# Kernel tuning notes

Measured on AMD Instinct MI355X. Metric: run time of the kernel, lower is better.

Reference implementation:

```python
import jax, jax.numpy as jnp
import numpy as np

B, S, C, H, D = 2, 2048, 1024, 16, 64  # hidden C must equal H*D (value is a reshape of key_states)


def setup_inputs() -> dict:
    key = jax.random.key(0)
    ks = jax.random.split(key, 7)
    query_states = jax.random.normal(ks[0], (B, S, C), dtype=jnp.float32)
    key_states = jax.random.normal(ks[1], (B, S, C), dtype=jnp.float32)
    attention_mask = jax.random.randint(ks[2], (B, 1, 1, S), 0, 2).astype(jnp.int32)
    Wq = jax.random.normal(ks[3], (C, H, D), dtype=jnp.float32) * 0.02
    bq = jnp.zeros((H, D), dtype=jnp.float32)
    Wk = jax.random.normal(ks[4], (C, H, D), dtype=jnp.float32) * 0.02
    bk = jnp.zeros((H, D), dtype=jnp.float32)
    return {
        "query_states": query_states,
        "key_states": key_states,
        "attention_mask": attention_mask,
        "Wq": Wq,
        "bq": bq,
        "Wk": Wk,
        "bk": bk,
    }


def reference(query_states, key_states, attention_mask, Wq, bq, Wk, bk):
    # EinsumDense 'abc,cde->abde' with bias on 'de'
    q = jnp.einsum("bsc,chd->bshd", query_states, Wq) + bq  # [B,S,H,D]
    k = jnp.einsum("bsc,chd->bshd", key_states, Wk) + bk    # [B,S,H,D]
    # value is just key_states reshaped into head layout (no projection!)
    v = key_states.reshape(k.shape)                          # [B,S,H,D]
    # scale query by 1/sqrt(dk)
    q = q * jax.lax.rsqrt(jnp.asarray(D, q.dtype))
    # 'aecd,abcd->acbe': a=batch, c=head, b=query pos, e=key pos
    scores = jnp.einsum("bkhd,bqhd->bhqk", k, q)             # [B,H,Sq,Sk]
    mask = (1.0 - attention_mask.astype(scores.dtype)) * -10000.0
    scores = scores + mask
    probs = jax.nn.softmax(scores, axis=-1)
    # dropout is identity at training=False (default)
    # 'acbe,aecd->abcd': weighted sum of values over key positions
    out = jnp.einsum("bhqk,bkhd->bqhd", probs, v)            # [B,S,H,D]
    return out
```

## Files before the change

### kernel.cpp

```cpp
#include <hip/hip_runtime.h>

#define BSZ 2
#define SEQ 2048
#define CH  1024
#define NH  16
#define HD  64
#define LOG2E 1.4426950408889634f
#define MASKC (-14426.950408889634f)

typedef short  bf16x8 __attribute__((ext_vector_type(8)));
typedef short  bf16x4 __attribute__((ext_vector_type(4)));
typedef float  f32x4  __attribute__((ext_vector_type(4)));

__device__ __forceinline__ short f2bf(float f) {
    union { float f; unsigned u; } v; v.f = f;
    unsigned r = v.u + 0x7FFFu + ((v.u >> 16) & 1u);
    return (short)(r >> 16);
}
__device__ __forceinline__ short f2bf_fast(float f) {
    union { float f; unsigned u; } v; v.f = f;
    return (short)((v.u + 0x8000u) >> 16);
}
__device__ __forceinline__ float exp2_hw(float x) {
#if __has_builtin(__builtin_amdgcn_exp2f)
    return __builtin_amdgcn_exp2f(x);
#else
    float r;
    asm volatile("v_exp_f32 %0, %1\n\ts_nop 1" : "=v"(r) : "v"(x));
    return r;
#endif
}

#if __has_builtin(__builtin_amdgcn_mfma_f32_16x16x16bf16_1k)
__device__ __forceinline__ f32x4 mfma16x16x16(bf16x4 a, bf16x4 b, f32x4 c) {
    return __builtin_amdgcn_mfma_f32_16x16x16bf16_1k(a, b, c, 0, 0, 0);
}
#else
__device__ __forceinline__ f32x4 mfma16x16x16(bf16x4 a, bf16x4 b, f32x4 c) {
    f32x4 d;
    asm("v_mfma_f32_16x16x16_bf16 %0, %1, %2, %3"
        : "=v"(d) : "v"(a), "v"(b), "v"(c));
    return d;
}
#endif

__global__ __launch_bounds__(256) void prep(
    const float* __restrict__ query, const float* __restrict__ key,
    const float* __restrict__ Wq, const float* __restrict__ Wk,
    short* __restrict__ qc, short* __restrict__ kc,
    short* __restrict__ wtq, short* __restrict__ wtk,
    short* __restrict__ vtr)
{
    __shared__ float tile[64][65];
    const int bid = blockIdx.x;
    const int tid = threadIdx.x;

    if (bid < 4096) {
        const float* s = (bid < 2048) ? query : key;
        short*       d = (bid < 2048) ? qc : kc;
        long i = ((long)(bid & 2047) * 256 + tid) * 8;
        float4 v0 = *(const float4*)&s[i];
        float4 v1 = *(const float4*)&s[i + 4];
        bf16x8 o;
        o[0] = f2bf(v0.x); o[1] = f2bf(v0.y); o[2] = f2bf(v0.z); o[3] = f2bf(v0.w);
        o[4] = f2bf(v1.x); o[5] = f2bf(v1.y); o[6] = f2bf(v1.z); o[7] = f2bf(v1.w);
        *(bf16x8*)&d[i] = o;
        return;
    }

    const float* s; short* d;
    int r0, c0, srs, drs;
    if (bid < 4608) {
        int t = bid - 4096;
        s   = (t < 256) ? Wq : Wk;
        d   = (t < 256) ? wtq : wtk;
        t  &= 255;
        r0  = (t >> 4) * 64;
        c0  = (t & 15) * 64;
        srs = CH; drs = CH;
    } else {
        int t = bid - 4608;
        int z = t >> 5;
        int sy = t & 31;
        s   = key + (long)(z >> 4) * SEQ * CH + (long)(z & 15) * HD;
        d   = vtr + (long)z * HD * SEQ;
        r0  = sy * 64;
        c0  = 0;
        srs = CH; drs = SEQ;
    }

    const int r  = tid >> 2;
    const int c4 = (tid & 3) << 4;
    #pragma unroll
    for (int i = 0; i < 16; i += 4) {
        float4 v = *(const float4*)&s[(long)(r0 + r) * srs + c0 + c4 + i];
        tile[r][c4 + i + 0] = v.x;
        tile[r][c4 + i + 1] = v.y;
        tile[r][c4 + i + 2] = v.z;
        tile[r][c4 + i + 3] = v.w;
    }
    __syncthreads();
    bf16x8 o0, o1;
    #pragma unroll
    for (int i = 0; i < 8; i++) o0[i] = f2bf(tile[c4 + i][r]);
    #pragma unroll
    for (int i = 0; i < 8; i++) o1[i] = f2bf(tile[c4 + 8 + i][r]);
    *(bf16x8*)&d[(long)(c0 + r) * drs + r0 + c4 + 0] = o0;
    *(bf16x8*)&d[(long)(c0 + r) * drs + r0 + c4 + 8] = o1;
}

__global__ __launch_bounds__(256, 2) void proj_mfma(
    const short* __restrict__ Xq, const short* __restrict__ Xk,
    const short* __restrict__ Wtq, const short* __restrict__ Wtk,
    const float* __restrict__ bq_, const float* __restrict__ bk_,
    short* __restrict__ Yq, short* __restrict__ Yk)
{
    __shared__ short At[2][128 * 72];
    __shared__ short Bt[2][128 * 72];

    const int bid  = blockIdx.x;
    const int g    = bid >> 3, xcd = bid & 7;
    const int pair = ((g >> 3) << 3) | xcd;
    const int xt   = g & 7;
    const int yy   = pair >> 1;
    const int zz   = pair & 1;

    const short* X    = zz ? Xk  : Xq;
    const short* Wt   = zz ? Wtk : Wtq;
    const float* bias = zz ? bk_ : bq_;
    short*       Y    = zz ? Yk  : Yq;
    const float scale = zz ? 1.0f : (0.125f * LOG2E);

    const int tid  = threadIdx.x;
    const int lane = tid & 63, w = tid >> 6;
    const int quad = lane >> 4, t16 = lane & 15;
    const int m0 = yy * 128, n0 = xt * 128;
    const int srow = tid >> 1;
    const int shalf = (tid & 1) * 32;

    f32x4 acc[4][4];
    #pragma unroll
    for (int i = 0; i < 4; i++)
        #pragma unroll
        for (int j = 0; j < 4; j++)
            acc[i][j] = (f32x4){0.f, 0.f, 0.f, 0.f};

    const int M0 = (w >> 1) * 64, N0 = (w & 1) * 64;
    const int NIT = CH / 64;

    bf16x8 ar[4], br[4];
    #pragma unroll
    for (int c = 0; c < 4; c++) {
        ar[c] = *(const bf16x8*)&X [(long)(m0 + srow) * CH + shalf + 8 * c];
        br[c] = *(const bf16x8*)&Wt[(long)(n0 + srow) * CH + shalf + 8 * c];
    }
    #pragma unroll
    for (int c = 0; c < 4; c++) {
        *(bf16x8*)&At[0][srow * 72 + shalf + 8 * c] = ar[c];
        *(bf16x8*)&Bt[0][srow * 72 + shalf + 8 * c] = br[c];
    }
    #pragma unroll
    for (int c = 0; c < 4; c++) {
        ar[c] = *(const bf16x8*)&X [(long)(m0 + srow) * CH + 64 + shalf + 8 * c];
        br[c] = *(const bf16x8*)&Wt[(long)(n0 + srow) * CH + 64 + shalf + 8 * c];
    }
    __syncthreads();

    for (int it = 0; it < NIT; it++) {
        const int buf = it & 1;
        if (it + 1 < NIT) {
            #pragma unroll
            for (int c = 0; c < 4; c++) {
                *(bf16x8*)&At[buf ^ 1][srow * 72 + shalf + 8 * c] = ar[c];
                *(bf16x8*)&Bt[buf ^ 1][srow * 72 + shalf + 8 * c] = br[c];
            }
            if (it + 2 < NIT) {
                const long ko = (long)(it + 2) * 64;
                #pragma unroll
                for (int c = 0; c < 4; c++) {
                    ar[c] = *(const bf16x8*)&X [(long)(m0 + srow) * CH + ko + shalf + 8 * c];
                    br[c] = *(const bf16x8*)&Wt[(long)(n0 + srow) * CH + ko + shalf + 8 * c];
                }
            }
        }

        #pragma unroll
        for (int kk = 0; kk < 2; kk++) {
            bf16x8 af[4], bw[4];
            #pragma unroll
            for (int im = 0; im < 4; im++)
                af[im] = *(bf16x8*)&At[buf][(M0 + 16 * im + t16) * 72 + kk * 32 + quad * 8];
            #pragma unroll
            for (int jn = 0; jn < 4; jn++)
                bw[jn] = *(bf16x8*)&Bt[buf][(N0 + 16 * jn + t16) * 72 + kk * 32 + quad * 8];
            #pragma unroll
            for (int im = 0; im < 4; im++)
                #pragma unroll
                for (int jn = 0; jn < 4; jn++)
                    acc[im][jn] = __builtin_amdgcn_mfma_f32_16x16x32_bf16(
                        af[im], bw[jn], acc[im][jn], 0, 0, 0);
        }
        __syncthreads();
    }

    #pragma unroll
    for (int jn = 0; jn < 4; jn++) {
        float bs = bias[n0 + N0 + 16 * jn + t16];
        #pragma unroll
        for (int im = 0; im < 4; im++)
            #pragma unroll
            for (int reg = 0; reg < 4; reg++) {
                float y = (acc[im][jn][reg] + bs) * scale;
                Y[(long)(m0 + M0 + 16 * im + 4 * quad + reg) * (NH * HD)
                  + n0 + N0 + 16 * jn + t16] = f2bf(y);
            }
    }
}

__global__ __launch_bounds__(256, 2) void attn_mfma(
    const short* __restrict__ qp,
    const short* __restrict__ kp,
    const short* __restrict__ vt,
    const int*   __restrict__ amask,
    float* __restrict__ out)
{
    __shared__ short Kt[2][64 * 72];
    __shared__ short Vt[2][64 * 72];
    __shared__ float Msk[SEQ];

    const int bid = blockIdx.x;
    const int g   = bid >> 3, xcd = bid & 7;
    const int hb  = ((g >> 4) << 3) | xcd;
    const int qt  = g & 15;

    const int qt0 = qt * 128;
    const int h   = hb & 15;
    const int b   = hb >> 4;
    const int tid = threadIdx.x;
    const int lane = tid & 63, w = tid >> 6;
    const int quad = lane >> 4, t16 = lane & 15;

    {
        int4 a0 = *(const int4*)&amask[b * SEQ + tid * 8];
        int4 a1 = *(const int4*)&amask[b * SEQ + tid * 8 + 4];
        float4 f0 = {a0.x ? 0.f : MASKC, a0.y ? 0.f : MASKC,
                     a0.z ? 0.f : MASKC, a0.w ? 0.f : MASKC};
        float4 f1 = {a1.x ? 0.f : MASKC, a1.y ? 0.f : MASKC,
                     a1.z ? 0.f : MASKC, a1.w ? 0.f : MASKC};
        *(float4*)&Msk[tid * 8]     = f0;
        *(float4*)&Msk[tid * 8 + 4] = f1;
    }

    bf16x8 qf[2][2];
    #pragma unroll
    for (int qm = 0; qm < 2; qm++)
        #pragma unroll
        for (int ds = 0; ds < 2; ds++)
            qf[qm][ds] = *(const bf16x8*)&qp[
                (long)(b * SEQ + qt0 + w * 32 + qm * 16 + t16) * CH
                + h * HD + ds * 32 + quad * 8];

    f32x4 oa[4][2];
    float l_r[2];
    #pragma unroll
    for (int dt = 0; dt < 4; dt++)
        #pragma unroll
        for (int qm = 0; qm < 2; qm++)
            oa[dt][qm] = (f32x4){0.f, 0.f, 0.f, 0.f};
    l_r[0] = l_r[1] = 0.f;

    const int srow  = tid >> 2;
    const int scol  = (tid & 3) * 16;
    const long kbase = (long)(b * SEQ) * CH + h * HD;
    const long vbase = ((long)(b * NH + h) * HD) * SEQ;
    const int NIT = SEQ / 64;

    bf16x8 kr[2], vr[2];
    #pragma unroll
    for (int c = 0; c < 2; c++) {
        kr[c] = *(const bf16x8*)&kp[kbase + (long)srow * CH + scol + 8 * c];
        vr[c] = *(const bf16x8*)&vt[vbase + (long)srow * SEQ + scol + 8 * c];
    }
    #pragma unroll
    for (int c = 0; c < 2; c++) {
        *(bf16x8*)&Kt[0][srow * 72 + scol + 8 * c] = kr[c];
        *(bf16x8*)&Vt[0][srow * 72 + scol + 8 * c] = vr[c];
    }
    #pragma unroll
    for (int c = 0; c < 2; c++) {
        kr[c] = *(const bf16x8*)&kp[kbase + (long)(64 + srow) * CH + scol + 8 * c];
        vr[c] = *(const bf16x8*)&vt[vbase + (long)srow * SEQ + 64 + scol + 8 * c];
    }
    __syncthreads();

    for (int it = 0; it < NIT; it++) {
        const int buf = it & 1;
        const int kt0 = it * 64;

        if (it + 1 < NIT) {
            #pragma unroll
            for (int c = 0; c < 2; c++) {
                *(bf16x8*)&Kt[buf ^ 1][srow * 72 + scol + 8 * c] = kr[c];
                *(bf16x8*)&Vt[buf ^ 1][srow * 72 + scol + 8 * c] = vr[c];
            }
            if (it + 2 < NIT) {
                const int kn = kt0 + 128;
                #pragma unroll
                for (int c = 0; c < 2; c++) {
                    kr[c] = *(const bf16x8*)&kp[kbase + (long)(kn + srow) * CH + scol + 8 * c];
                    vr[c] = *(const bf16x8*)&vt[vbase + (long)srow * SEQ + kn + scol + 8 * c];
                }
            }
        }

        float4 mv4[4];
        #pragma unroll
        for (int jt = 0; jt < 4; jt++)
            mv4[jt] = *(const float4*)&Msk[kt0 + jt * 16 + quad * 4];

        f32x4 sa[2][4];
        #pragma unroll
        for (int qm = 0; qm < 2; qm++)
            #pragma unroll
            for (int jt = 0; jt < 4; jt++)
                sa[qm][jt] = (f32x4){mv4[jt].x, mv4[jt].y, mv4[jt].z, mv4[jt].w};
        #pragma unroll
        for (int ds = 0; ds < 2; ds++) {
            bf16x8 kb[4];
            #pragma unroll
            for (int jt = 0; jt < 4; jt++)
                kb[jt] = *(bf16x8*)&Kt[buf][(jt * 16 + t16) * 72 + ds * 32 + quad * 8];
            __builtin_amdgcn_s_setprio(1);
            #pragma unroll
            for (int qm = 0; qm < 2; qm++)
                #pragma unroll
                for (int jt = 0; jt < 4; jt++)
                    sa[qm][jt] = __builtin_amdgcn_mfma_f32_16x16x32_bf16(
                        kb[jt], qf[qm][ds], sa[qm][jt], 0, 0, 0);
            __builtin_amdgcn_s_setprio(0);
        }

        #pragma unroll
        for (int jt = 0; jt < 4; jt++) {
            bf16x4 pbq[2];
            #pragma unroll
            for (int qm = 0; qm < 2; qm++) {
                float p0 = exp2_hw(sa[qm][jt][0]);
                float p1 = exp2_hw(sa[qm][jt][1]);
                float p2 = exp2_hw(sa[qm][jt][2]);
                float p3 = exp2_hw(sa[qm][jt][3]);
                l_r[qm] += (p0 + p1) + (p2 + p3);
                bf16x4 pk;
                pk[0] = f2bf_fast(p0); pk[1] = f2bf_fast(p1);
                pk[2] = f2bf_fast(p2); pk[3] = f2bf_fast(p3);
                pbq[qm] = pk;
            }
            bf16x4 va[4];
            #pragma unroll
            for (int dt = 0; dt < 4; dt++)
                va[dt] = *(bf16x4*)&Vt[buf][(dt * 16 + t16) * 72 + jt * 16 + quad * 4];
            __builtin_amdgcn_s_setprio(1);
            #pragma unroll
            for (int dt = 0; dt < 4; dt++)
                #pragma unroll
                for (int qm = 0; qm < 2; qm++)
                    oa[dt][qm] = mfma16x16x16(va[dt], pbq[qm], oa[dt][qm]);
            __builtin_amdgcn_s_setprio(0);
        }
        __syncthreads();
    }

    #pragma unroll
    for (int qm = 0; qm < 2; qm++) {
        float l = l_r[qm];
        l += __shfl_xor(l, 16, 64);
        l += __shfl_xor(l, 32, 64);
        float inv = 1.0f / l;
        int q = qt0 + w * 32 + qm * 16 + t16;
        #pragma unroll
        for (int dt = 0; dt < 4; dt++) {
            f32x4 o = oa[dt][qm];
            float4 st = {o[0] * inv, o[1] * inv, o[2] * inv, o[3] * inv};
            *(float4*)&out[((long)(b * SEQ + q) * NH + h) * HD + dt * 16 + quad * 4] = st;
        }
    }
}

extern "C" void kernel_launch(void* const* d_in, const int* in_sizes, int n_in,
                              void* d_out, int out_size, void* d_ws, size_t ws_size,
                              hipStream_t stream) {
    const float* query = (const float*)d_in[0];
    const float* key   = (const float*)d_in[1];
    const int*   amask = (const int*)d_in[2];
    const float* Wq    = (const float*)d_in[3];
    const float* bq    = (const float*)d_in[4];
    const float* Wk    = (const float*)d_in[5];
    const float* bk    = (const float*)d_in[6];
    float* out = (float*)d_out;

    char* ws = (char*)d_ws;
    const long MB = 1024 * 1024;
    short* qc  = (short*)(ws + 0 * MB);
    short* kc  = (short*)(ws + 8 * MB);
    short* qp  = (short*)(ws + 16 * MB);
    short* kp  = (short*)(ws + 24 * MB);
    short* vtr = (short*)(ws + 32 * MB);
    short* wtq = (short*)(ws + 40 * MB);
    short* wtk = (short*)(ws + 42 * MB);

    prep<<<dim3(5632), 256, 0, stream>>>(query, key, Wq, Wk, qc, kc, wtq, wtk, vtr);

    proj_mfma<<<dim3(512), 256, 0, stream>>>(qc, kc, wtq, wtk, bq, bk, qp, kp);

    attn_mfma<<<dim3(512), 256, 0, stream>>>(qp, kp, vtr, amask, out);
}
```

Baseline: 170.8 us.

## Load K and V fragments directly from global memory, dropping LDS staging

Removes the double-buffered shared-memory tiles for K and V. Each wave now loads its MFMA operand fragments straight from global memory into registers. K for the next tile is prefetched into a ping-pong register set while the current tile computes, and V fragments are loaded at the top of each iteration. This eliminates LDS writes, LDS reads and per-iteration __syncthreads. The cost is that the four waves of a block redundantly fetch the same K/V tiles through L2/L1, with less-coalesced 8/16-byte row-strided accesses, and register pressure rises.

```diff
diff --git a/kernel.cpp b/kernel.cpp
--- a/kernel.cpp
+++ b/kernel.cpp
@@ -224,8 +224,6 @@
     const int*   __restrict__ amask,
     float* __restrict__ out)
 {
-    __shared__ short Kt[2][64 * 72];
-    __shared__ short Vt[2][64 * 72];
     __shared__ float Msk[SEQ];
 
     const int bid = blockIdx.x;
@@ -269,49 +267,34 @@
             oa[dt][qm] = (f32x4){0.f, 0.f, 0.f, 0.f};
     l_r[0] = l_r[1] = 0.f;
 
-    const int srow  = tid >> 2;
-    const int scol  = (tid & 3) * 16;
     const long kbase = (long)(b * SEQ) * CH + h * HD;
     const long vbase = ((long)(b * NH + h) * HD) * SEQ;
     const int NIT = SEQ / 64;
 
-    bf16x8 kr[2], vr[2];
-    #pragma unroll
-    for (int c = 0; c < 2; c++) {
-        kr[c] = *(const bf16x8*)&kp[kbase + (long)srow * CH + scol + 8 * c];
-        vr[c] = *(const bf16x8*)&vt[vbase + (long)srow * SEQ + scol + 8 * c];
-    }
-    #pragma unroll
-    for (int c = 0; c < 2; c++) {
-        *(bf16x8*)&Kt[0][srow * 72 + scol + 8 * c] = kr[c];
-        *(bf16x8*)&Vt[0][srow * 72 + scol + 8 * c] = vr[c];
-    }
-    #pragma unroll
-    for (int c = 0; c < 2; c++) {
-        kr[c] = *(const bf16x8*)&kp[kbase + (long)(64 + srow) * CH + scol + 8 * c];
-        vr[c] = *(const bf16x8*)&vt[vbase + (long)srow * SEQ + 64 + scol + 8 * c];
-    }
     __syncthreads();
 
-    for (int it = 0; it < NIT; it++) {
-        const int buf = it & 1;
+    auto loadKB = [&](bf16x8 (&kb)[2][4], int kt0) {
+        #pragma unroll
+        for (int ds = 0; ds < 2; ds++)
+            #pragma unroll
+            for (int jt = 0; jt < 4; jt++)
+                kb[ds][jt] = *(const bf16x8*)&kp[
+                    kbase + (long)(kt0 + jt * 16 + t16) * CH + ds * 32 + quad * 8];
+    };
+
+    bf16x8 kbA[2][4], kbB[2][4];
+    loadKB(kbA, 0);
+
+    auto body = [&](bf16x8 (&kbC)[2][4], bf16x8 (&kbN)[2][4], int it) {
         const int kt0 = it * 64;
 
-        if (it + 1 < NIT) {
-            #pragma unroll
-            for (int c = 0; c < 2; c++) {
-                *(bf16x8*)&Kt[buf ^ 1][srow * 72 + scol + 8 * c] = kr[c];
-                *(bf16x8*)&Vt[buf ^ 1][srow * 72 + scol + 8 * c] = vr[c];
-            }
-            if (it + 2 < NIT) {
-                const int kn = kt0 + 128;
-                #pragma unroll
-                for (int c = 0; c < 2; c++) {
-                    kr[c] = *(const bf16x8*)&kp[kbase + (long)(kn + srow) * CH + scol + 8 * c];
-                    vr[c] = *(const bf16x8*)&vt[vbase + (long)srow * SEQ + kn + scol + 8 * c];
-                }
-            }
-        }
+        bf16x4 va[4][4];
+        #pragma unroll
+        for (int dt = 0; dt < 4; dt++)
+            #pragma unroll
+            for (int jt = 0; jt < 4; jt++)
+                va[dt][jt] = *(const bf16x4*)&vt[
+                    vbase + (long)(dt * 16 + t16) * SEQ + kt0 + jt * 16 + quad * 4];
 
         float4 mv4[4];
         #pragma unroll
@@ -326,19 +309,17 @@
                 sa[qm][jt] = (f32x4){mv4[jt].x, mv4[jt].y, mv4[jt].z, mv4[jt].w};
         #pragma unroll
         for (int ds = 0; ds < 2; ds++) {
-            bf16x8 kb[4];
-            #pragma unroll
-            for (int jt = 0; jt < 4; jt++)
-                kb[jt] = *(bf16x8*)&Kt[buf][(jt * 16 + t16) * 72 + ds * 32 + quad * 8];
             __builtin_amdgcn_s_setprio(1);
             #pragma unroll
             for (int qm = 0; qm < 2; qm++)
                 #pragma unroll
                 for (int jt = 0; jt < 4; jt++)
                     sa[qm][jt] = __builtin_amdgcn_mfma_f32_16x16x32_bf16(
-                        kb[jt], qf[qm][ds], sa[qm][jt], 0, 0, 0);
+                        kbC[ds][jt], qf[qm][ds], sa[qm][jt], 0, 0, 0);
             __builtin_amdgcn_s_setprio(0);
         }
+
+        if (it + 1 < NIT) loadKB(kbN, kt0 + 64);
 
         #pragma unroll
         for (int jt = 0; jt < 4; jt++) {
@@ -355,19 +336,20 @@
                 pk[2] = f2bf_fast(p2); pk[3] = f2bf_fast(p3);
                 pbq[qm] = pk;
             }
-            bf16x4 va[4];
-            #pragma unroll
-            for (int dt = 0; dt < 4; dt++)
-                va[dt] = *(bf16x4*)&Vt[buf][(dt * 16 + t16) * 72 + jt * 16 + quad * 4];
             __builtin_amdgcn_s_setprio(1);
             #pragma unroll
             for (int dt = 0; dt < 4; dt++)
                 #pragma unroll
                 for (int qm = 0; qm < 2; qm++)
-                    oa[dt][qm] = mfma16x16x16(va[dt], pbq[qm], oa[dt][qm]);
+                    oa[dt][qm] = mfma16x16x16(va[dt][jt], pbq[qm], oa[dt][qm]);
             __builtin_amdgcn_s_setprio(0);
         }
-        __syncthreads();
+    };
+
+    #pragma unroll 1
+    for (int itp = 0; itp < NIT; itp += 2) {
+        body(kbA, kbB, itp);
+        body(kbB, kbA, itp + 1);
     }
 
     #pragma unroll
```

Result: slower. 292.1 us (+71.1%).

## Load V fragments directly from global into registers and use hardware bf16 pack

Applied to the files above, without the earlier changes.

Removes the LDS staging buffer for V. Each lane now loads its V operand fragments straight from global memory at the start of every iteration, dropping the V shared-memory writes and reads and cutting LDS usage. The manual float-to-bf16 rounding of probabilities is replaced with v_cvt_pk_bf16_f32 inline asm, which does round-to-nearest-even in hardware. The trade-off is uncoalesced 8-byte global loads that are issued each iteration without double-buffered prefetch, which can expose memory latency and raise register pressure.

```diff
diff --git a/kernel.cpp b/kernel.cpp
--- a/kernel.cpp
+++ b/kernel.cpp
@@ -16,10 +16,6 @@
     union { float f; unsigned u; } v; v.f = f;
     unsigned r = v.u + 0x7FFFu + ((v.u >> 16) & 1u);
     return (short)(r >> 16);
-}
-__device__ __forceinline__ short f2bf_fast(float f) {
-    union { float f; unsigned u; } v; v.f = f;
-    return (short)((v.u + 0x8000u) >> 16);
 }
 __device__ __forceinline__ float exp2_hw(float x) {
 #if __has_builtin(__builtin_amdgcn_exp2f)
@@ -29,6 +25,18 @@
     asm volatile("v_exp_f32 %0, %1\n\ts_nop 1" : "=v"(r) : "v"(x));
     return r;
 #endif
+}
+
+__device__ __forceinline__ bf16x4 pack4_rne(float p0, float p1, float p2, float p3) {
+    unsigned lo, hi;
+    asm("s_nop 1\n\t"
+        "v_cvt_pk_bf16_f32 %0, %2, %3\n\t"
+        "v_cvt_pk_bf16_f32 %1, %4, %5"
+        : "=&v"(lo), "=&v"(hi)
+        : "v"(p0), "v"(p1), "v"(p2), "v"(p3));
+    union { unsigned u[2]; bf16x4 v; } r;
+    r.u[0] = lo; r.u[1] = hi;
+    return r.v;
 }
 
 #if __has_builtin(__builtin_amdgcn_mfma_f32_16x16x16bf16_1k)
@@ -225,7 +233,6 @@
     float* __restrict__ out)
 {
     __shared__ short Kt[2][64 * 72];
-    __shared__ short Vt[2][64 * 72];
     __shared__ float Msk[SEQ];
 
     const int bid = blockIdx.x;
@@ -275,41 +282,39 @@
     const long vbase = ((long)(b * NH + h) * HD) * SEQ;
     const int NIT = SEQ / 64;
 
-    bf16x8 kr[2], vr[2];
-    #pragma unroll
-    for (int c = 0; c < 2; c++) {
+    bf16x8 kr[2];
+    #pragma unroll
+    for (int c = 0; c < 2; c++)
         kr[c] = *(const bf16x8*)&kp[kbase + (long)srow * CH + scol + 8 * c];
-        vr[c] = *(const bf16x8*)&vt[vbase + (long)srow * SEQ + scol + 8 * c];
-    }
-    #pragma unroll
-    for (int c = 0; c < 2; c++) {
+    #pragma unroll
+    for (int c = 0; c < 2; c++)
         *(bf16x8*)&Kt[0][srow * 72 + scol + 8 * c] = kr[c];
-        *(bf16x8*)&Vt[0][srow * 72 + scol + 8 * c] = vr[c];
-    }
-    #pragma unroll
-    for (int c = 0; c < 2; c++) {
+    #pragma unroll
+    for (int c = 0; c < 2; c++)
         kr[c] = *(const bf16x8*)&kp[kbase + (long)(64 + srow) * CH + scol + 8 * c];
-        vr[c] = *(const bf16x8*)&vt[vbase + (long)srow * SEQ + 64 + scol + 8 * c];
-    }
     __syncthreads();
 
     for (int it = 0; it < NIT; it++) {
         const int buf = it & 1;
         const int kt0 = it * 64;
 
+        bf16x4 va[4][4];
+        #pragma unroll
+        for (int dt = 0; dt < 4; dt++)
+            #pragma unroll
+            for (int jt = 0; jt < 4; jt++)
+                va[dt][jt] = *(const bf16x4*)&vt[
+                    vbase + (long)(dt * 16 + t16) * SEQ + kt0 + jt * 16 + quad * 4];
+
         if (it + 1 < NIT) {
             #pragma unroll
-            for (int c = 0; c < 2; c++) {
+            for (int c = 0; c < 2; c++)
                 *(bf16x8*)&Kt[buf ^ 1][srow * 72 + scol + 8 * c] = kr[c];
-                *(bf16x8*)&Vt[buf ^ 1][srow * 72 + scol + 8 * c] = vr[c];
-            }
             if (it + 2 < NIT) {
-                const int kn = kt0 + 128;
                 #pragma unroll
-                for (int c = 0; c < 2; c++) {
-                    kr[c] = *(const bf16x8*)&kp[kbase + (long)(kn + srow) * CH + scol + 8 * c];
-                    vr[c] = *(const bf16x8*)&vt[vbase + (long)srow * SEQ + kn + scol + 8 * c];
-                }
+                for (int c = 0; c < 2; c++)
+                    kr[c] = *(const bf16x8*)&kp[
+                        kbase + (long)(kt0 + 128 + srow) * CH + scol + 8 * c];
             }
         }
 
@@ -350,21 +355,14 @@
                 float p2 = exp2_hw(sa[qm][jt][2]);
                 float p3 = exp2_hw(sa[qm][jt][3]);
                 l_r[qm] += (p0 + p1) + (p2 + p3);
-                bf16x4 pk;
-                pk[0] = f2bf_fast(p0); pk[1] = f2bf_fast(p1);
-                pk[2] = f2bf_fast(p2); pk[3] = f2bf_fast(p3);
-                pbq[qm] = pk;
+                pbq[qm] = pack4_rne(p0, p1, p2, p3);
             }
-            bf16x4 va[4];
-            #pragma unroll
-            for (int dt = 0; dt < 4; dt++)
-                va[dt] = *(bf16x4*)&Vt[buf][(dt * 16 + t16) * 72 + jt * 16 + quad * 4];
             __builtin_amdgcn_s_setprio(1);
             #pragma unroll
             for (int dt = 0; dt < 4; dt++)
                 #pragma unroll
                 for (int qm = 0; qm < 2; qm++)
-                    oa[dt][qm] = mfma16x16x16(va[dt], pbq[qm], oa[dt][qm]);
+                    oa[dt][qm] = mfma16x16x16(va[dt][jt], pbq[qm], oa[dt][qm]);
             __builtin_amdgcn_s_setprio(0);
         }
         __syncthreads();
```

Result: slower. 247.1 us (+44.7%).
